# Kernel optimization log

Hardware: AMD Instinct MI355X
Metric: run time of the kernel (lower is better)

## Reference

```python
import jax, jax.numpy as jnp
import numpy as np

N_GRAPHS = 256
RATIO = 0.5


def setup_inputs() -> dict:
    key = jax.random.key(0)
    k0, k1, k2, k3, k4 = jax.random.split(key, 5)
    N, E, D = 100000, 1600000, 64
    x = jax.random.normal(k0, (N, D), dtype=jnp.float32)
    edge_index = jax.random.randint(k1, (2, E), 0, N, dtype=jnp.int32)
    batch = jnp.sort(jax.random.randint(k2, (N,), 0, N_GRAPHS, dtype=jnp.int32))
    # GraphConv(in_channels=64, out_channels=1) parameters
    w_rel = jax.random.normal(k3, (D,), dtype=jnp.float32) * 0.1
    b_rel = jnp.zeros((), dtype=jnp.float32)
    w_root = jax.random.normal(k4, (D,), dtype=jnp.float32) * 0.1
    return {"x": x, "edge_index": edge_index, "batch": batch,
            "w_rel": w_rel, "b_rel": b_rel, "w_root": w_root}


def reference(x, edge_index, batch, w_rel, b_rel, w_root):
    N = x.shape[0]
    src, dst = edge_index[0], edge_index[1]
    # GraphConv score: lin_rel(sum_{j in N(i)} x_j) + lin_root(x_i)
    agg = jax.ops.segment_sum(x[src], dst, num_segments=N)        # [N, D]
    score = jnp.tanh(agg @ w_rel + b_rel + x @ w_root)            # [N], SAGPool tanh
    # per-graph topk: keep k_g = ceil(ratio * n_g) highest-score nodes
    sizes = jax.ops.segment_sum(jnp.ones(N, jnp.int32), batch,
                                num_segments=N_GRAPHS)            # [G]
    k = jnp.ceil(RATIO * sizes.astype(jnp.float32)).astype(jnp.int32)
    starts = jnp.concatenate([jnp.zeros(1, jnp.int32),
                              jnp.cumsum(sizes)[:-1].astype(jnp.int32)])
    order = jnp.lexsort((-score, batch))                          # graph-major, score desc
    rank = jnp.arange(N, dtype=jnp.int32) - starts[batch[order]]  # rank within graph
    keep_sorted = rank < k[batch[order]]
    keep = jnp.zeros(N, dtype=bool).at[order].set(keep_sorted)
    # kept nodes are scaled by their tanh score; dropped nodes contribute 0
    w = jnp.where(keep, score, jnp.zeros_like(score))             # [N]
    num = jax.ops.segment_sum(x * w[:, None], batch, num_segments=N_GRAPHS)
    cnt = jax.ops.segment_sum(keep.astype(x.dtype), batch, num_segments=N_GRAPHS)
    return num / jnp.maximum(cnt, 1.0)[:, None]                   # global_mean_pool
```

## Files before the change

kernel.cpp:

```cpp
#include <hip/hip_runtime.h>

#define NGRAPHS 256
#define CHUNK 4096
#define BINR 256
#define CAPB 6144
#define MAXB 512
#define NMAX 2048

__global__ __launch_bounds__(512) void k1_fused(
    const float* __restrict__ x,
    const int*   __restrict__ batch,
    const int*   __restrict__ ei,
    const float* __restrict__ w_rel,
    const float* __restrict__ w_root,
    float* __restrict__ p, float* __restrict__ r,
    int* __restrict__ starts, int* __restrict__ ends,
    int* __restrict__ C,
    int N, int E, int NBLKE, int NBINS, int vecE)
{
    __shared__ int hist[MAXB];
    int tid = threadIdx.x;

    if ((int)blockIdx.x < NBLKE) {
        for (int b = tid; b < NBINS; b += 512) hist[b] = 0;
        __syncthreads();
        int beg = blockIdx.x * CHUNK;
        int end = min(beg + CHUNK, E);
        if (vecE) {
            const int4* d4 = (const int4*)(ei + E);
            for (int i = (beg >> 2) + tid; i < (end >> 2); i += 512) {
                int4 d = d4[i];
                atomicAdd(&hist[d.x >> 8], 1);
                atomicAdd(&hist[d.y >> 8], 1);
                atomicAdd(&hist[d.z >> 8], 1);
                atomicAdd(&hist[d.w >> 8], 1);
            }
        } else {
            for (int i = beg + tid; i < end; i += 512)
                atomicAdd(&hist[ei[E + i] >> 8], 1);
        }
        __syncthreads();
        for (int b = tid; b < NBINS; b += 512)
            C[(size_t)blockIdx.x * NBINS + b] = hist[b];
        return;
    }

    int row = ((int)blockIdx.x - NBLKE) * 32 + (tid >> 4);
    int fq  = tid & 15;
    if (row >= N) return;
    if (fq == 0) {
        int b = batch[row];
        if (row == 0) {
            for (int g = 0; g < b; ++g) { starts[g] = 0; ends[g] = 0; }
            starts[b] = 0;
        } else {
            int bp = batch[row - 1];
            if (bp != b) {
                ends[bp] = row;
                for (int g = bp + 1; g < b; ++g) { starts[g] = row; ends[g] = row; }
                starts[b] = row;
            }
        }
        if (row == N - 1) {
            ends[b] = N;
            for (int g = b + 1; g < NGRAPHS; ++g) { starts[g] = N; ends[g] = N; }
        }
    }
    float4 v  = *(const float4*)(x + (size_t)row * 64 + fq * 4);
    float4 wr = ((const float4*)w_rel)[fq];
    float4 wo = ((const float4*)w_root)[fq];
    float a = v.x * wr.x + v.y * wr.y + v.z * wr.z + v.w * wr.w;
    float c = v.x * wo.x + v.y * wo.y + v.z * wo.z + v.w * wo.w;
    a += __shfl_down(a, 8); c += __shfl_down(c, 8);
    a += __shfl_down(a, 4); c += __shfl_down(c, 4);
    a += __shfl_down(a, 2); c += __shfl_down(c, 2);
    a += __shfl_down(a, 1); c += __shfl_down(c, 1);
    if (fq == 0) { p[row] = a; r[row] = c; }
}

__global__ __launch_bounds__(512) void kA2_scan(
    int* __restrict__ C, int* __restrict__ cursor, int NBLK, int NBINS)
{
    __shared__ int sh[512];
    int b = blockIdx.x;
    int t = threadIdx.x;
    int c = (t < NBLK) ? C[(size_t)t * NBINS + b] : 0;
    sh[t] = c;
    __syncthreads();
    #pragma unroll
    for (int off = 1; off < 512; off <<= 1) {
        int v = (t >= off) ? sh[t - off] : 0;
        __syncthreads();
        sh[t] += v;
        __syncthreads();
    }
    if (t < NBLK) C[(size_t)t * NBINS + b] = b * CAPB + (sh[t] - c);
    if (t == 511) cursor[b] = sh[t];
}

__global__ __launch_bounds__(512) void kA3_scatter(
    const int* __restrict__ ei,
    const int* __restrict__ C,
    unsigned* __restrict__ bucket,
    int E, int NBINS, int vecE)
{
    __shared__ int cur[MAXB];
    int tid = threadIdx.x;
    for (int b = tid; b < NBINS; b += 512)
        cur[b] = C[(size_t)blockIdx.x * NBINS + b];
    __syncthreads();
    int beg = blockIdx.x * CHUNK;
    int end = min(beg + CHUNK, E);
    if (vecE) {
        const int4* s4 = (const int4*)ei;
        const int4* d4 = (const int4*)(ei + E);
        for (int i = (beg >> 2) + tid; i < (end >> 2); i += 512) {
            int4 d = d4[i];
            int4 s = s4[i];
            int b0 = d.x >> 8, p0 = atomicAdd(&cur[b0], 1);
            if (p0 < (b0 + 1) * CAPB) bucket[p0] = ((unsigned)s.x << 8) | (unsigned)(d.x & 255);
            int b1 = d.y >> 8, p1 = atomicAdd(&cur[b1], 1);
            if (p1 < (b1 + 1) * CAPB) bucket[p1] = ((unsigned)s.y << 8) | (unsigned)(d.y & 255);
            int b2 = d.z >> 8, p2 = atomicAdd(&cur[b2], 1);
            if (p2 < (b2 + 1) * CAPB) bucket[p2] = ((unsigned)s.z << 8) | (unsigned)(d.z & 255);
            int b3 = d.w >> 8, p3 = atomicAdd(&cur[b3], 1);
            if (p3 < (b3 + 1) * CAPB) bucket[p3] = ((unsigned)s.w << 8) | (unsigned)(d.w & 255);
        }
    } else {
        for (int i = beg + tid; i < end; i += 512) {
            int d = ei[E + i];
            int s = ei[i];
            int b = d >> 8;
            int pos = atomicAdd(&cur[b], 1);
            if (pos < (b + 1) * CAPB)
                bucket[pos] = ((unsigned)s << 8) | (unsigned)(d & 255);
        }
    }
}

__global__ __launch_bounds__(512) void kB_score(
    const unsigned* __restrict__ bucket,
    const int* __restrict__ cursor,
    const float* __restrict__ p,
    const float* __restrict__ r,
    const float* __restrict__ brel,
    float* __restrict__ score, int N)
{
    __shared__ float acc[BINR];
    int tid = threadIdx.x;
    int b   = blockIdx.x;
    if (tid < BINR) acc[tid] = 0.0f;
    __syncthreads();
    int lo  = b * CAPB;
    int cnt = min(cursor[b], CAPB);
    const uint4* bk4 = (const uint4*)(bucket + lo);
    int quart = cnt >> 2;
    for (int e = tid; e < quart; e += 512) {
        uint4 u = bk4[e];
        float v0 = p[u.x >> 8], v1 = p[u.y >> 8];
        float v2 = p[u.z >> 8], v3 = p[u.w >> 8];
        atomicAdd(&acc[u.x & 255u], v0);
        atomicAdd(&acc[u.y & 255u], v1);
        atomicAdd(&acc[u.z & 255u], v2);
        atomicAdd(&acc[u.w & 255u], v3);
    }
    int tail = cnt & 3;
    if (tid < tail) {
        unsigned u = bucket[lo + (quart << 2) + tid];
        atomicAdd(&acc[u & 255u], p[u >> 8]);
    }
    __syncthreads();
    int node = b * BINR + tid;
    if (tid < BINR && node < N)
        score[node] = tanhf(acc[tid] + brel[0] + r[node]);
}

__global__ __launch_bounds__(256) void kZ_zero(float* __restrict__ a, int N)
{
    int i = blockIdx.x * 256 + threadIdx.x;
    if (i < N) a[i] = 0.0f;
}
__global__ __launch_bounds__(256) void k2_scatter(
    const int* __restrict__ ei, const float* __restrict__ p,
    float* aggdot, int E)
{
    int i = blockIdx.x * 256 + threadIdx.x;
    if (i < E) unsafeAtomicAdd(&aggdot[ei[E + i]], p[ei[i]]);
}
__global__ __launch_bounds__(256) void kS_score(
    const float* __restrict__ aggdot, const float* __restrict__ r,
    const float* __restrict__ brel, float* __restrict__ score, int N)
{
    int i = blockIdx.x * 256 + threadIdx.x;
    if (i < N) score[i] = tanhf(aggdot[i] + brel[0] + r[i]);
}

__global__ __launch_bounds__(512) void k4_pool(
    const float* __restrict__ x,
    const float* __restrict__ score,
    const int* __restrict__ starts,
    const int* __restrict__ ends,
    float* __restrict__ out)
{
    __shared__ __align__(16) float sc[NMAX];
    __shared__ int   kidx[NMAX / 2 + 64];
    __shared__ float kw[NMAX / 2 + 64];
    __shared__ float accs[8][64][4];
    __shared__ int   pctr;

    int g   = blockIdx.x;
    int tid = threadIdx.x;
    int start = starts[g];
    int n     = ends[g] - start;
    if (n > NMAX) n = NMAX;
    int k = (n + 1) >> 1;
    if (tid == 0) pctr = 0;

    for (int i = tid; i < n; i += 512) sc[i] = score[start + i];
    __syncthreads();

    int n4 = n & ~3;
    for (int i = tid; i < n; i += 512) {
        float si = sc[i];
        int rank = 0;
        int j = 0;
        for (; j < n4; j += 4) {
            float4 s4 = *(const float4*)&sc[j];
            rank += (s4.x > si) || (s4.x == si && (j + 0) < i);
            rank += (s4.y > si) || (s4.y == si && (j + 1) < i);
            rank += (s4.z > si) || (s4.z == si && (j + 2) < i);
            rank += (s4.w > si) || (s4.w == si && (j + 3) < i);
        }
        for (; j < n; ++j) {
            float sj = sc[j];
            rank += (sj > si) || (sj == si && j < i);
        }
        if (rank < k) {
            int pos = atomicAdd(&pctr, 1);
            kidx[pos] = i;
            kw[pos]   = si;
        }
    }
    __syncthreads();
    int k32 = (k + 31) & ~31;
    for (int e = k + tid; e < k32; e += 512) { kidx[e] = 0; kw[e] = 0.0f; }
    __syncthreads();

    int wg   = tid >> 6;
    int lane = tid & 63;
    int rgrp = lane >> 4;
    int fq   = lane & 15;
    float a0 = 0.0f, a1 = 0.0f, a2 = 0.0f, a3 = 0.0f;
    #pragma unroll 2
    for (int e = wg * 4 + rgrp; e < k32; e += 32) {
        float wv = kw[e];
        int row  = start + kidx[e];
        const float4 v = *(const float4*)(x + (size_t)row * 64 + fq * 4);
        a0 += v.x * wv; a1 += v.y * wv; a2 += v.z * wv; a3 += v.w * wv;
    }
    accs[wg][lane][0] = a0; accs[wg][lane][1] = a1;
    accs[wg][lane][2] = a2; accs[wg][lane][3] = a3;
    __syncthreads();
    if (tid < 64) {
        int f = tid;
        float sum = 0.0f;
        #pragma unroll
        for (int gg = 0; gg < 8; ++gg)
            #pragma unroll
            for (int rg = 0; rg < 4; ++rg)
                sum += accs[gg][rg * 16 + (f >> 2)][f & 3];
        out[(size_t)g * 64 + f] = sum / fmaxf((float)k, 1.0f);
    }
}

extern "C" void kernel_launch(void* const* d_in, const int* in_sizes, int n_in,
                              void* d_out, int out_size, void* d_ws, size_t ws_size,
                              hipStream_t stream) {
    const float* x      = (const float*)d_in[0];
    const int*   ei     = (const int*)  d_in[1];
    const int*   batch  = (const int*)  d_in[2];
    const float* w_rel  = (const float*)d_in[3];
    const float* b_rel  = (const float*)d_in[4];
    const float* w_root = (const float*)d_in[5];
    float* out = (float*)d_out;

    int N = in_sizes[2];
    int E = in_sizes[1] / 2;
    int NBLKE = (E + CHUNK - 1) / CHUNK;
    int NBINS = (N + BINR - 1) / BINR;
    int vecE  = ((E & 3) == 0);

    float* p      = (float*)d_ws;
    float* r      = p + (size_t)N;
    float* score  = r + (size_t)N;
    int*   starts = (int*)(score + (size_t)N);
    int*   ends   = starts + NGRAPHS;
    int*   cursor = ends + NGRAPHS;
    int*   C      = cursor + MAXB;
    unsigned* bucket = (unsigned*)(C + (size_t)NBLKE * NBINS);
    size_t need = ((size_t)3 * N + 2 * NGRAPHS + MAXB
                   + (size_t)NBLKE * NBINS + (size_t)NBINS * CAPB) * 4;

    bool binned = (need <= ws_size) && (NBLKE <= 512) && (NBINS <= MAXB)
                  && (N < (1 << 24));

    int dotblks = (N + 31) / 32;
    if (binned) {
        k1_fused<<<NBLKE + dotblks, 512, 0, stream>>>(x, batch, ei, w_rel, w_root,
                                                      p, r, starts, ends, C,
                                                      N, E, NBLKE, NBINS, vecE);
        kA2_scan<<<NBINS, 512, 0, stream>>>(C, cursor, NBLKE, NBINS);
        kA3_scatter<<<NBLKE, 512, 0, stream>>>(ei, C, bucket, E, NBINS, vecE);
        kB_score<<<NBINS, 512, 0, stream>>>(bucket, cursor, p, r, b_rel, score, N);
    } else {
        float* aggdot = (float*)C;
        k1_fused<<<dotblks, 512, 0, stream>>>(x, batch, ei, w_rel, w_root,
                                              p, r, starts, ends, C, N, E, 0,
                                              NBINS, vecE);
        kZ_zero<<<(N + 255) / 256, 256, 0, stream>>>(aggdot, N);
        k2_scatter<<<(E + 255) / 256, 256, 0, stream>>>(ei, p, aggdot, E);
        kS_score<<<(N + 255) / 256, 256, 0, stream>>>(aggdot, r, b_rel, score, N);
    }
    k4_pool<<<NGRAPHS, 512, 0, stream>>>(x, score, starts, ends, out);
}
```

Baseline: 133.0 us.

## Bin edges by destination graph and fuse score aggregation into pooling kernel

Replaces the histogram/scan/scatter/score pipeline of node-range bins with a single scatter kernel. It stages edges in shared memory, bins them by the destination node's graph and reserves global space with atomics on per-graph cursors. The score aggregation and tanh now run inside the per-graph pool kernel, so the separate score kernel and the score array round-trip disappear. The cost is a random batch[] lookup per edge, fixed per-graph capacity (CAPG) that silently drops overflow edges, local index clamping at NMAX, and a 256-block pool kernel that now also does the edge reduction.

```diff
diff --git a/kernel.cpp b/kernel.cpp
--- a/kernel.cpp
+++ b/kernel.cpp
@@ -1,51 +1,22 @@
 #include <hip/hip_runtime.h>
 
 #define NGRAPHS 256
-#define CHUNK 4096
-#define BINR 256
-#define CAPB 6144
-#define MAXB 512
-#define NMAX 2048
-
-__global__ __launch_bounds__(512) void k1_fused(
+#define CHUNK   2048
+#define CAPG    12288
+#define NMAX    2048
+
+__global__ __launch_bounds__(512) void k1_dot(
     const float* __restrict__ x,
     const int*   __restrict__ batch,
-    const int*   __restrict__ ei,
     const float* __restrict__ w_rel,
     const float* __restrict__ w_root,
     float* __restrict__ p, float* __restrict__ r,
     int* __restrict__ starts, int* __restrict__ ends,
-    int* __restrict__ C,
-    int N, int E, int NBLKE, int NBINS, int vecE)
-{
-    __shared__ int hist[MAXB];
+    int* __restrict__ cursor, int N)
+{
     int tid = threadIdx.x;
-
-    if ((int)blockIdx.x < NBLKE) {
-        for (int b = tid; b < NBINS; b += 512) hist[b] = 0;
-        __syncthreads();
-        int beg = blockIdx.x * CHUNK;
-        int end = min(beg + CHUNK, E);
-        if (vecE) {
-            const int4* d4 = (const int4*)(ei + E);
-            for (int i = (beg >> 2) + tid; i < (end >> 2); i += 512) {
-                int4 d = d4[i];
-                atomicAdd(&hist[d.x >> 8], 1);
-                atomicAdd(&hist[d.y >> 8], 1);
-                atomicAdd(&hist[d.z >> 8], 1);
-                atomicAdd(&hist[d.w >> 8], 1);
-            }
-        } else {
-            for (int i = beg + tid; i < end; i += 512)
-                atomicAdd(&hist[ei[E + i] >> 8], 1);
-        }
-        __syncthreads();
-        for (int b = tid; b < NBINS; b += 512)
-            C[(size_t)blockIdx.x * NBINS + b] = hist[b];
-        return;
-    }
-
-    int row = ((int)blockIdx.x - NBLKE) * 32 + (tid >> 4);
+    if (blockIdx.x == 0 && tid < NGRAPHS) cursor[tid] = 0;
+    int row = (int)blockIdx.x * 32 + (tid >> 4);
     int fq  = tid & 15;
     if (row >= N) return;
     if (fq == 0) {
@@ -78,131 +49,110 @@
     if (fq == 0) { p[row] = a; r[row] = c; }
 }
 
-__global__ __launch_bounds__(512) void kA2_scan(
-    int* __restrict__ C, int* __restrict__ cursor, int NBLK, int NBINS)
-{
-    __shared__ int sh[512];
-    int b = blockIdx.x;
-    int t = threadIdx.x;
-    int c = (t < NBLK) ? C[(size_t)t * NBINS + b] : 0;
-    sh[t] = c;
-    __syncthreads();
-    #pragma unroll
-    for (int off = 1; off < 512; off <<= 1) {
-        int v = (t >= off) ? sh[t - off] : 0;
-        __syncthreads();
-        sh[t] += v;
-        __syncthreads();
-    }
-    if (t < NBLK) C[(size_t)t * NBINS + b] = b * CAPB + (sh[t] - c);
-    if (t == 511) cursor[b] = sh[t];
-}
-
-__global__ __launch_bounds__(512) void kA3_scatter(
+__global__ __launch_bounds__(512) void kSc_scatter(
     const int* __restrict__ ei,
-    const int* __restrict__ C,
+    const int* __restrict__ batch,
+    const int* __restrict__ starts,
+    int* __restrict__ cursor,
     unsigned* __restrict__ bucket,
-    int E, int NBINS, int vecE)
-{
-    __shared__ int cur[MAXB];
+    int E, int vecE)
+{
+    __shared__ __align__(16) unsigned stage[CHUNK];
+    __shared__ unsigned char sbin[CHUNK];
+    __shared__ int hist[NGRAPHS];
+    __shared__ int wb[NGRAPHS];
+    __shared__ int sst[NGRAPHS];
+
     int tid = threadIdx.x;
-    for (int b = tid; b < NBINS; b += 512)
-        cur[b] = C[(size_t)blockIdx.x * NBINS + b];
-    __syncthreads();
-    int beg = blockIdx.x * CHUNK;
+    if (tid < NGRAPHS) { hist[tid] = 0; sst[tid] = starts[tid]; }
+    __syncthreads();
+
+    int beg = (int)blockIdx.x * CHUNK;
     int end = min(beg + CHUNK, E);
     if (vecE) {
         const int4* s4 = (const int4*)ei;
         const int4* d4 = (const int4*)(ei + E);
         for (int i = (beg >> 2) + tid; i < (end >> 2); i += 512) {
+            int4 s = s4[i];
             int4 d = d4[i];
-            int4 s = s4[i];
-            int b0 = d.x >> 8, p0 = atomicAdd(&cur[b0], 1);
-            if (p0 < (b0 + 1) * CAPB) bucket[p0] = ((unsigned)s.x << 8) | (unsigned)(d.x & 255);
-            int b1 = d.y >> 8, p1 = atomicAdd(&cur[b1], 1);
-            if (p1 < (b1 + 1) * CAPB) bucket[p1] = ((unsigned)s.y << 8) | (unsigned)(d.y & 255);
-            int b2 = d.z >> 8, p2 = atomicAdd(&cur[b2], 1);
-            if (p2 < (b2 + 1) * CAPB) bucket[p2] = ((unsigned)s.z << 8) | (unsigned)(d.z & 255);
-            int b3 = d.w >> 8, p3 = atomicAdd(&cur[b3], 1);
-            if (p3 < (b3 + 1) * CAPB) bucket[p3] = ((unsigned)s.w << 8) | (unsigned)(d.w & 255);
+            int o = (i << 2) - beg;
+            int g0 = batch[d.x], g1 = batch[d.y], g2 = batch[d.z], g3 = batch[d.w];
+            int l0 = min(d.x - sst[g0], NMAX - 1);
+            int l1 = min(d.y - sst[g1], NMAX - 1);
+            int l2 = min(d.z - sst[g2], NMAX - 1);
+            int l3 = min(d.w - sst[g3], NMAX - 1);
+            uint4 st; uchar4 sb;
+            st.x = ((unsigned)s.x << 11) | (unsigned)l0; sb.x = (unsigned char)g0;
+            st.y = ((unsigned)s.y << 11) | (unsigned)l1; sb.y = (unsigned char)g1;
+            st.z = ((unsigned)s.z << 11) | (unsigned)l2; sb.z = (unsigned char)g2;
+            st.w = ((unsigned)s.w << 11) | (unsigned)l3; sb.w = (unsigned char)g3;
+            *(uint4*)&stage[o] = st;
+            *(uchar4*)&sbin[o] = sb;
+            atomicAdd(&hist[g0], 1);
+            atomicAdd(&hist[g1], 1);
+            atomicAdd(&hist[g2], 1);
+            atomicAdd(&hist[g3], 1);
         }
     } else {
         for (int i = beg + tid; i < end; i += 512) {
+            int s = ei[i];
             int d = ei[E + i];
-            int s = ei[i];
-            int b = d >> 8;
-            int pos = atomicAdd(&cur[b], 1);
-            if (pos < (b + 1) * CAPB)
-                bucket[pos] = ((unsigned)s << 8) | (unsigned)(d & 255);
-        }
-    }
-}
-
-__global__ __launch_bounds__(512) void kB_score(
-    const unsigned* __restrict__ bucket,
-    const int* __restrict__ cursor,
+            int g = batch[d];
+            int l = min(d - sst[g], NMAX - 1);
+            int o = i - beg;
+            stage[o] = ((unsigned)s << 11) | (unsigned)l;
+            sbin[o]  = (unsigned char)g;
+            atomicAdd(&hist[g], 1);
+        }
+    }
+    __syncthreads();
+    if (tid < NGRAPHS) {
+        int h = hist[tid];
+        wb[tid] = (h > 0) ? tid * CAPG + atomicAdd(&cursor[tid], h) : 0;
+    }
+    __syncthreads();
+    int cnt = end - beg;
+    for (int o = tid; o < cnt; o += 512) {
+        int b = sbin[o];
+        int pos = atomicAdd(&wb[b], 1);
+        if (pos < (b + 1) * CAPG) bucket[pos] = stage[o];
+    }
+}
+
+__global__ __launch_bounds__(256) void kZ_zero(float* __restrict__ a, int N)
+{
+    int i = blockIdx.x * 256 + threadIdx.x;
+    if (i < N) a[i] = 0.0f;
+}
+__global__ __launch_bounds__(256) void k2_scatter(
+    const int* __restrict__ ei, const float* __restrict__ p,
+    float* aggdot, int E)
+{
+    int i = blockIdx.x * 256 + threadIdx.x;
+    if (i < E) unsafeAtomicAdd(&aggdot[ei[E + i]], p[ei[i]]);
+}
+__global__ __launch_bounds__(256) void kS_score(
+    const float* __restrict__ aggdot, const float* __restrict__ r,
+    const float* __restrict__ brel, float* __restrict__ score, int N)
+{
+    int i = blockIdx.x * 256 + threadIdx.x;
+    if (i < N) score[i] = tanhf(aggdot[i] + brel[0] + r[i]);
+}
+
+__global__ __launch_bounds__(512) void kPool(
+    const float* __restrict__ x,
     const float* __restrict__ p,
     const float* __restrict__ r,
     const float* __restrict__ brel,
-    float* __restrict__ score, int N)
-{
-    __shared__ float acc[BINR];
-    int tid = threadIdx.x;
-    int b   = blockIdx.x;
-    if (tid < BINR) acc[tid] = 0.0f;
-    __syncthreads();
-    int lo  = b * CAPB;
-    int cnt = min(cursor[b], CAPB);
-    const uint4* bk4 = (const uint4*)(bucket + lo);
-    int quart = cnt >> 2;
-    for (int e = tid; e < quart; e += 512) {
-        uint4 u = bk4[e];
-        float v0 = p[u.x >> 8], v1 = p[u.y >> 8];
-        float v2 = p[u.z >> 8], v3 = p[u.w >> 8];
-        atomicAdd(&acc[u.x & 255u], v0);
-        atomicAdd(&acc[u.y & 255u], v1);
-        atomicAdd(&acc[u.z & 255u], v2);
-        atomicAdd(&acc[u.w & 255u], v3);
-    }
-    int tail = cnt & 3;
-    if (tid < tail) {
-        unsigned u = bucket[lo + (quart << 2) + tid];
-        atomicAdd(&acc[u & 255u], p[u >> 8]);
-    }
-    __syncthreads();
-    int node = b * BINR + tid;
-    if (tid < BINR && node < N)
-        score[node] = tanhf(acc[tid] + brel[0] + r[node]);
-}
-
-__global__ __launch_bounds__(256) void kZ_zero(float* __restrict__ a, int N)
-{
-    int i = blockIdx.x * 256 + threadIdx.x;
-    if (i < N) a[i] = 0.0f;
-}
-__global__ __launch_bounds__(256) void k2_scatter(
-    const int* __restrict__ ei, const float* __restrict__ p,
-    float* aggdot, int E)
-{
-    int i = blockIdx.x * 256 + threadIdx.x;
-    if (i < E) unsafeAtomicAdd(&aggdot[ei[E + i]], p[ei[i]]);
-}
-__global__ __launch_bounds__(256) void kS_score(
-    const float* __restrict__ aggdot, const float* __restrict__ r,
-    const float* __restrict__ brel, float* __restrict__ score, int N)
-{
-    int i = blockIdx.x * 256 + threadIdx.x;
-    if (i < N) score[i] = tanhf(aggdot[i] + brel[0] + r[i]);
-}
-
-__global__ __launch_bounds__(512) void k4_pool(
-    const float* __restrict__ x,
-    const float* __restrict__ score,
+    const unsigned* __restrict__ bucket,
+    const int* __restrict__ cursor,
     const int* __restrict__ starts,
     const int* __restrict__ ends,
+    const float* __restrict__ score_g,
     float* __restrict__ out)
 {
     __shared__ __align__(16) float sc[NMAX];
+    __shared__ float acc[NMAX];
     __shared__ int   kidx[NMAX / 2 + 64];
     __shared__ float kw[NMAX / 2 + 64];
     __shared__ float accs[8][64][4];
@@ -216,7 +166,34 @@
     int k = (n + 1) >> 1;
     if (tid == 0) pctr = 0;
 
-    for (int i = tid; i < n; i += 512) sc[i] = score[start + i];
+    if (score_g) {
+        for (int i = tid; i < n; i += 512) sc[i] = score_g[start + i];
+    } else {
+        for (int i = tid; i < n; i += 512) acc[i] = 0.0f;
+        __syncthreads();
+        int lo  = g * CAPG;
+        int cnt = min(cursor[g], CAPG);
+        const uint4* bk4 = (const uint4*)(bucket + lo);
+        int quart = cnt >> 2;
+        for (int e = tid; e < quart; e += 512) {
+            uint4 u = bk4[e];
+            float v0 = p[u.x >> 11], v1 = p[u.y >> 11];
+            float v2 = p[u.z >> 11], v3 = p[u.w >> 11];
+            atomicAdd(&acc[u.x & 2047u], v0);
+            atomicAdd(&acc[u.y & 2047u], v1);
+            atomicAdd(&acc[u.z & 2047u], v2);
+            atomicAdd(&acc[u.w & 2047u], v3);
+        }
+        int tail = cnt & 3;
+        if (tid < tail) {
+            unsigned u = bucket[lo + (quart << 2) + tid];
+            atomicAdd(&acc[u & 2047u], p[u >> 11]);
+        }
+        __syncthreads();
+        float bb = brel[0];
+        for (int i = tid; i < n; i += 512)
+            sc[i] = tanhf(acc[i] + bb + r[start + i]);
+    }
     __syncthreads();
 
     int n4 = n & ~3;
@@ -262,14 +239,13 @@
     accs[wg][lane][2] = a2; accs[wg][lane][3] = a3;
     __syncthreads();
     if (tid < 64) {
-        int f = tid;
         float sum = 0.0f;
         #pragma unroll
         for (int gg = 0; gg < 8; ++gg)
             #pragma unroll
             for (int rg = 0; rg < 4; ++rg)
-                sum += accs[gg][rg * 16 + (f >> 2)][f & 3];
-        out[(size_t)g * 64 + f] = sum / fmaxf((float)k, 1.0f);
+                sum += accs[gg][rg * 16 + (tid >> 2)][tid & 3];
+        out[(size_t)g * 64 + tid] = sum / fmaxf((float)k, 1.0f);
     }
 }
 
@@ -287,39 +263,35 @@
     int N = in_sizes[2];
     int E = in_sizes[1] / 2;
     int NBLKE = (E + CHUNK - 1) / CHUNK;
-    int NBINS = (N + BINR - 1) / BINR;
     int vecE  = ((E & 3) == 0);
+    int dotblks = (N + 31) / 32;
 
     float* p      = (float*)d_ws;
     float* r      = p + (size_t)N;
-    float* score  = r + (size_t)N;
-    int*   starts = (int*)(score + (size_t)N);
+    int*   starts = (int*)(r + (size_t)N);
     int*   ends   = starts + NGRAPHS;
     int*   cursor = ends + NGRAPHS;
-    int*   C      = cursor + MAXB;
-    unsigned* bucket = (unsigned*)(C + (size_t)NBLKE * NBINS);
-    size_t need = ((size_t)3 * N + 2 * NGRAPHS + MAXB
-                   + (size_t)NBLKE * NBINS + (size_t)NBINS * CAPB) * 4;
-
-    bool binned = (need <= ws_size) && (NBLKE <= 512) && (NBINS <= MAXB)
-                  && (N < (1 << 24));
-
-    int dotblks = (N + 31) / 32;
+    size_t boff = (size_t)2 * N + 3 * NGRAPHS;
+    boff = (boff + 3) & ~(size_t)3;
+    unsigned* bucket = (unsigned*)d_ws + boff;
+    size_t need = (boff + (size_t)NGRAPHS * CAPG) * 4;
+
+    bool binned = (need <= ws_size) && (N < (1 << 17));
+
+    k1_dot<<<dotblks, 512, 0, stream>>>(x, batch, w_rel, w_root,
+                                        p, r, starts, ends, cursor, N);
     if (binned) {
-        k1_fused<<<NBLKE + dotblks, 512, 0, stream>>>(x, batch, ei, w_rel, w_root,
-                                                      p, r, starts, ends, C,
-                                                      N, E, NBLKE, NBINS, vecE);
-        kA2_scan<<<NBINS, 512, 0, stream>>>(C, cursor, NBLKE, NBINS);
-        kA3_scatter<<<NBLKE, 512, 0, stream>>>(ei, C, bucket, E, NBINS, vecE);
-        kB_score<<<NBINS, 512, 0, stream>>>(bucket, cursor, p, r, b_rel, score, N);
+        kSc_scatter<<<NBLKE, 512, 0, stream>>>(ei, batch, starts, cursor,
+                                               bucket, E, vecE);
+        kPool<<<NGRAPHS, 512, 0, stream>>>(x, p, r, b_rel, bucket, cursor,
+                                           starts, ends, nullptr, out);
     } else {
-        float* aggdot = (float*)C;
-        k1_fused<<<dotblks, 512, 0, stream>>>(x, batch, ei, w_rel, w_root,
-                                              p, r, starts, ends, C, N, E, 0,
-                                              NBINS, vecE);
+        float* score  = (float*)(cursor + NGRAPHS);
+        float* aggdot = score + (size_t)N;
         kZ_zero<<<(N + 255) / 256, 256, 0, stream>>>(aggdot, N);
         k2_scatter<<<(E + 255) / 256, 256, 0, stream>>>(ei, p, aggdot, E);
         kS_score<<<(N + 255) / 256, 256, 0, stream>>>(aggdot, r, b_rel, score, N);
-    }
-    k4_pool<<<NGRAPHS, 512, 0, stream>>>(x, score, starts, ends, out);
-}
+        kPool<<<NGRAPHS, 512, 0, stream>>>(x, p, r, b_rel, nullptr, nullptr,
+                                           starts, ends, score, out);
+    }
+}
```

Measured after the change: 138.7 us. +4.3%, slower.

## Halve bin width, fix edge-chunk count, and use per-bin serial scan

Applied to the files above, without the earlier changes.

Destination bins shrink from 256 to 128 nodes, doubling the number of score-accumulation blocks. The edge histogram and scatter now use a fixed count of 512 chunks instead of 4096-edge chunks. The per-bin tree scan is replaced by one thread per bin walking all chunks serially, which reads coalesced across bins. The aim is more parallelism in the scoring stage and cheaper scan synchronization, at the risk of a latency-bound serial scan loop and more, smaller bins.

```diff
diff --git a/kernel.cpp b/kernel.cpp
--- a/kernel.cpp
+++ b/kernel.cpp
@@ -1,11 +1,11 @@
 #include <hip/hip_runtime.h>
 
 #define NGRAPHS 256
-#define CHUNK 4096
-#define BINR 256
-#define CAPB 6144
-#define MAXB 512
-#define NMAX 2048
+#define BINR  128
+#define CAPB  3072
+#define MAXB  1024
+#define NBLKC 512
+#define NMAX  2048
 
 __global__ __launch_bounds__(512) void k1_fused(
     const float* __restrict__ x,
@@ -16,36 +16,37 @@
     float* __restrict__ p, float* __restrict__ r,
     int* __restrict__ starts, int* __restrict__ ends,
     int* __restrict__ C,
-    int N, int E, int NBLKE, int NBINS, int vecE)
+    int N, int E, int chunkE, int NBINSP, int vecE)
 {
     __shared__ int hist[MAXB];
     int tid = threadIdx.x;
 
-    if ((int)blockIdx.x < NBLKE) {
-        for (int b = tid; b < NBINS; b += 512) hist[b] = 0;
+    if ((int)blockIdx.x < NBLKC) {
+        if (E <= 0) return;
+        for (int b = tid; b < NBINSP; b += 512) hist[b] = 0;
         __syncthreads();
-        int beg = blockIdx.x * CHUNK;
-        int end = min(beg + CHUNK, E);
+        int beg = (int)blockIdx.x * chunkE;
+        int end = min(beg + chunkE, E);
         if (vecE) {
             const int4* d4 = (const int4*)(ei + E);
             for (int i = (beg >> 2) + tid; i < (end >> 2); i += 512) {
                 int4 d = d4[i];
-                atomicAdd(&hist[d.x >> 8], 1);
-                atomicAdd(&hist[d.y >> 8], 1);
-                atomicAdd(&hist[d.z >> 8], 1);
-                atomicAdd(&hist[d.w >> 8], 1);
+                atomicAdd(&hist[d.x >> 7], 1);
+                atomicAdd(&hist[d.y >> 7], 1);
+                atomicAdd(&hist[d.z >> 7], 1);
+                atomicAdd(&hist[d.w >> 7], 1);
             }
         } else {
             for (int i = beg + tid; i < end; i += 512)
-                atomicAdd(&hist[ei[E + i] >> 8], 1);
+                atomicAdd(&hist[ei[E + i] >> 7], 1);
         }
         __syncthreads();
-        for (int b = tid; b < NBINS; b += 512)
-            C[(size_t)blockIdx.x * NBINS + b] = hist[b];
+        for (int b = tid; b < NBINSP; b += 512)
+            C[(size_t)blockIdx.x * NBINSP + b] = hist[b];
         return;
     }
 
-    int row = ((int)blockIdx.x - NBLKE) * 32 + (tid >> 4);
+    int row = ((int)blockIdx.x - NBLKC) * 32 + (tid >> 4);
     int fq  = tid & 15;
     if (row >= N) return;
     if (fq == 0) {
@@ -78,62 +79,59 @@
     if (fq == 0) { p[row] = a; r[row] = c; }
 }
 
-__global__ __launch_bounds__(512) void kA2_scan(
-    int* __restrict__ C, int* __restrict__ cursor, int NBLK, int NBINS)
-{
-    __shared__ int sh[512];
-    int b = blockIdx.x;
-    int t = threadIdx.x;
-    int c = (t < NBLK) ? C[(size_t)t * NBINS + b] : 0;
-    sh[t] = c;
-    __syncthreads();
-    #pragma unroll
-    for (int off = 1; off < 512; off <<= 1) {
-        int v = (t >= off) ? sh[t - off] : 0;
-        __syncthreads();
-        sh[t] += v;
-        __syncthreads();
-    }
-    if (t < NBLK) C[(size_t)t * NBINS + b] = b * CAPB + (sh[t] - c);
-    if (t == 511) cursor[b] = sh[t];
+__global__ __launch_bounds__(64) void kA2_scan(
+    int* __restrict__ C, int* __restrict__ cursor, int NBLK, int NBINSP)
+{
+    int b = (int)blockIdx.x * 64 + threadIdx.x;
+    if (b >= NBINSP) return;
+    int run  = 0;
+    int base = b * CAPB;
+    #pragma unroll 4
+    for (int e = 0; e < NBLK; ++e) {
+        size_t idx = (size_t)e * NBINSP + b;
+        int c = C[idx];
+        C[idx] = base + run;
+        run += c;
+    }
+    cursor[b] = run;
 }
 
 __global__ __launch_bounds__(512) void kA3_scatter(
     const int* __restrict__ ei,
     const int* __restrict__ C,
     unsigned* __restrict__ bucket,
-    int E, int NBINS, int vecE)
+    int E, int chunkE, int NBINSP, int vecE)
 {
     __shared__ int cur[MAXB];
     int tid = threadIdx.x;
-    for (int b = tid; b < NBINS; b += 512)
-        cur[b] = C[(size_t)blockIdx.x * NBINS + b];
-    __syncthreads();
-    int beg = blockIdx.x * CHUNK;
-    int end = min(beg + CHUNK, E);
+    for (int b = tid; b < NBINSP; b += 512)
+        cur[b] = C[(size_t)blockIdx.x * NBINSP + b];
+    __syncthreads();
+    int beg = (int)blockIdx.x * chunkE;
+    int end = min(beg + chunkE, E);
     if (vecE) {
         const int4* s4 = (const int4*)ei;
         const int4* d4 = (const int4*)(ei + E);
         for (int i = (beg >> 2) + tid; i < (end >> 2); i += 512) {
             int4 d = d4[i];
             int4 s = s4[i];
-            int b0 = d.x >> 8, p0 = atomicAdd(&cur[b0], 1);
-            if (p0 < (b0 + 1) * CAPB) bucket[p0] = ((unsigned)s.x << 8) | (unsigned)(d.x & 255);
-            int b1 = d.y >> 8, p1 = atomicAdd(&cur[b1], 1);
-            if (p1 < (b1 + 1) * CAPB) bucket[p1] = ((unsigned)s.y << 8) | (unsigned)(d.y & 255);
-            int b2 = d.z >> 8, p2 = atomicAdd(&cur[b2], 1);
-            if (p2 < (b2 + 1) * CAPB) bucket[p2] = ((unsigned)s.z << 8) | (unsigned)(d.z & 255);
-            int b3 = d.w >> 8, p3 = atomicAdd(&cur[b3], 1);
-            if (p3 < (b3 + 1) * CAPB) bucket[p3] = ((unsigned)s.w << 8) | (unsigned)(d.w & 255);
+            int b0 = d.x >> 7, p0 = atomicAdd(&cur[b0], 1);
+            if (p0 < (b0 + 1) * CAPB) bucket[p0] = ((unsigned)s.x << 7) | (unsigned)(d.x & 127);
+            int b1 = d.y >> 7, p1 = atomicAdd(&cur[b1], 1);
+            if (p1 < (b1 + 1) * CAPB) bucket[p1] = ((unsigned)s.y << 7) | (unsigned)(d.y & 127);
+            int b2 = d.z >> 7, p2 = atomicAdd(&cur[b2], 1);
+            if (p2 < (b2 + 1) * CAPB) bucket[p2] = ((unsigned)s.z << 7) | (unsigned)(d.z & 127);
+            int b3 = d.w >> 7, p3 = atomicAdd(&cur[b3], 1);
+            if (p3 < (b3 + 1) * CAPB) bucket[p3] = ((unsigned)s.w << 7) | (unsigned)(d.w & 127);
         }
     } else {
         for (int i = beg + tid; i < end; i += 512) {
             int d = ei[E + i];
             int s = ei[i];
-            int b = d >> 8;
+            int b = d >> 7;
             int pos = atomicAdd(&cur[b], 1);
             if (pos < (b + 1) * CAPB)
-                bucket[pos] = ((unsigned)s << 8) | (unsigned)(d & 255);
+                bucket[pos] = ((unsigned)s << 7) | (unsigned)(d & 127);
         }
     }
 }
@@ -157,17 +155,17 @@
     int quart = cnt >> 2;
     for (int e = tid; e < quart; e += 512) {
         uint4 u = bk4[e];
-        float v0 = p[u.x >> 8], v1 = p[u.y >> 8];
-        float v2 = p[u.z >> 8], v3 = p[u.w >> 8];
-        atomicAdd(&acc[u.x & 255u], v0);
-        atomicAdd(&acc[u.y & 255u], v1);
-        atomicAdd(&acc[u.z & 255u], v2);
-        atomicAdd(&acc[u.w & 255u], v3);
+        float v0 = p[u.x >> 7], v1 = p[u.y >> 7];
+        float v2 = p[u.z >> 7], v3 = p[u.w >> 7];
+        atomicAdd(&acc[u.x & 127u], v0);
+        atomicAdd(&acc[u.y & 127u], v1);
+        atomicAdd(&acc[u.z & 127u], v2);
+        atomicAdd(&acc[u.w & 127u], v3);
     }
     int tail = cnt & 3;
     if (tid < tail) {
         unsigned u = bucket[lo + (quart << 2) + tid];
-        atomicAdd(&acc[u & 255u], p[u >> 8]);
+        atomicAdd(&acc[u & 127u], p[u >> 7]);
     }
     __syncthreads();
     int node = b * BINR + tid;
@@ -262,14 +260,13 @@
     accs[wg][lane][2] = a2; accs[wg][lane][3] = a3;
     __syncthreads();
     if (tid < 64) {
-        int f = tid;
         float sum = 0.0f;
         #pragma unroll
         for (int gg = 0; gg < 8; ++gg)
             #pragma unroll
             for (int rg = 0; rg < 4; ++rg)
-                sum += accs[gg][rg * 16 + (f >> 2)][f & 3];
-        out[(size_t)g * 64 + f] = sum / fmaxf((float)k, 1.0f);
+                sum += accs[gg][rg * 16 + (tid >> 2)][tid & 3];
+        out[(size_t)g * 64 + tid] = sum / fmaxf((float)k, 1.0f);
     }
 }
 
@@ -286,9 +283,11 @@
 
     int N = in_sizes[2];
     int E = in_sizes[1] / 2;
-    int NBLKE = (E + CHUNK - 1) / CHUNK;
-    int NBINS = (N + BINR - 1) / BINR;
-    int vecE  = ((E & 3) == 0);
+    int NBINS  = (N + BINR - 1) / BINR;
+    int NBINSP = (NBINS + 15) & ~15;
+    int chunkE = (((E + NBLKC - 1) / NBLKC) + 3) & ~3;
+    int vecE   = ((E & 3) == 0);
+    int dotblks = (N + 31) / 32;
 
     float* p      = (float*)d_ws;
     float* r      = p + (size_t)N;
@@ -297,26 +296,25 @@
     int*   ends   = starts + NGRAPHS;
     int*   cursor = ends + NGRAPHS;
     int*   C      = cursor + MAXB;
-    unsigned* bucket = (unsigned*)(C + (size_t)NBLKE * NBINS);
-    size_t need = ((size_t)3 * N + 2 * NGRAPHS + MAXB
-                   + (size_t)NBLKE * NBINS + (size_t)NBINS * CAPB) * 4;
-
-    bool binned = (need <= ws_size) && (NBLKE <= 512) && (NBINS <= MAXB)
-                  && (N < (1 << 24));
-
-    int dotblks = (N + 31) / 32;
+    size_t boff = (size_t)3 * N + 2 * NGRAPHS + MAXB + (size_t)NBLKC * NBINSP;
+    boff = (boff + 3) & ~(size_t)3;
+    unsigned* bucket = (unsigned*)d_ws + boff;
+    size_t need = (boff + (size_t)NBINSP * CAPB) * 4;
+
+    bool binned = (need <= ws_size) && (NBINSP <= MAXB) && (N <= (1 << 24));
+
     if (binned) {
-        k1_fused<<<NBLKE + dotblks, 512, 0, stream>>>(x, batch, ei, w_rel, w_root,
-                                                      p, r, starts, ends, C,
-                                                      N, E, NBLKE, NBINS, vecE);
-        kA2_scan<<<NBINS, 512, 0, stream>>>(C, cursor, NBLKE, NBINS);
-        kA3_scatter<<<NBLKE, 512, 0, stream>>>(ei, C, bucket, E, NBINS, vecE);
+        k1_fused<<<NBLKC + dotblks, 512, 0, stream>>>(
+            x, batch, ei, w_rel, w_root, p, r, starts, ends, C,
+            N, E, chunkE, NBINSP, vecE);
+        kA2_scan<<<(NBINSP + 63) / 64, 64, 0, stream>>>(C, cursor, NBLKC, NBINSP);
+        kA3_scatter<<<NBLKC, 512, 0, stream>>>(ei, C, bucket, E, chunkE, NBINSP, vecE);
         kB_score<<<NBINS, 512, 0, stream>>>(bucket, cursor, p, r, b_rel, score, N);
     } else {
         float* aggdot = (float*)C;
-        k1_fused<<<dotblks, 512, 0, stream>>>(x, batch, ei, w_rel, w_root,
-                                              p, r, starts, ends, C, N, E, 0,
-                                              NBINS, vecE);
+        k1_fused<<<NBLKC + dotblks, 512, 0, stream>>>(
+            x, batch, ei, w_rel, w_root, p, r, starts, ends, C,
+            N, 0, 0, NBINSP, vecE);
         kZ_zero<<<(N + 255) / 256, 256, 0, stream>>>(aggdot, N);
         k2_scatter<<<(E + 255) / 256, 256, 0, stream>>>(ei, p, aggdot, E);
         kS_score<<<(N + 255) / 256, 256, 0, stream>>>(aggdot, r, b_rel, score, N);
```

Result: slower. 201.5 us (+51.5%).
